# Optimization experiments

Measured on AMD Instinct MI355X. Metric: run time of the kernel, lower is better.

## Reference

```python
import jax, jax.numpy as jnp
import numpy as np

BATCH, T, VOCAB, HIDDEN = 32, 256, 8192, 1024
SCALE = 0.02  # small init so logits stay sane through the recurrence


def setup_inputs() -> dict:
    key = jax.random.key(0)
    ks = jax.random.split(key, 4)
    inputs = jax.random.normal(ks[0], (BATCH, T, VOCAB), dtype=jnp.float32)
    Wi = jax.random.normal(ks[1], (VOCAB, 4 * HIDDEN), dtype=jnp.float32) * SCALE
    Wh = jax.random.normal(ks[2], (HIDDEN, 4 * HIDDEN), dtype=jnp.float32) * SCALE
    bh = jnp.zeros((4 * HIDDEN,), dtype=jnp.float32)
    Wp = jax.random.normal(ks[3], (HIDDEN, VOCAB), dtype=jnp.float32) * SCALE
    bp = jnp.zeros((VOCAB,), dtype=jnp.float32)
    c0 = jnp.zeros((BATCH, HIDDEN), dtype=jnp.float32)
    h0 = jnp.zeros((BATCH, HIDDEN), dtype=jnp.float32)
    return {"inputs": inputs, "Wi": Wi, "Wh": Wh, "bh": bh,
            "Wp": Wp, "bp": bp, "c0": c0, "h0": h0}


def _decode(inputs, Wi, Wh, bh, Wp, bp, c0, h0, rng):
    vocab = inputs.shape[2]

    def step(carry, x_t):
        rng, c, h, last_pred = carry
        rng, cat_rng = jax.random.split(rng)
        x = last_pred  # teacher_force=False: feed back sampled one-hot token
        # fused LSTM gates (flax gate order i, f, g, o)
        z = x @ Wi + h @ Wh + bh  # [B, 4H]
        i, f, g, o = jnp.split(z, 4, axis=-1)
        c = jax.nn.sigmoid(f) * c + jax.nn.sigmoid(i) * jnp.tanh(g)
        h = jax.nn.sigmoid(o) * jnp.tanh(c)
        logits = h @ Wp + bp  # [B, V]
        tok = jax.random.categorical(cat_rng, logits)  # [B] int
        pred = jax.nn.one_hot(tok, vocab, dtype=jnp.float32)  # [B, V]
        return (rng, c, h, pred), (logits, pred)

    init = (rng, c0, h0, inputs[:, 0])
    xs = jnp.swapaxes(inputs, 0, 1)  # [T, B, V]
    _, (logits, preds) = jax.lax.scan(step, init, xs)
    # scan stacks on axis 0; original scan_in_dim puts time back on axis 1
    return jnp.swapaxes(logits, 0, 1), jnp.swapaxes(preds, 0, 1)


def reference(inputs, Wi, Wh, bh, Wp, bp, c0, h0):
    rng = jax.random.key(42)  # stands in for self.make_rng('lstm')
    return _decode(inputs, Wi, Wh, bh, Wp, bp, c0, h0, rng)
```

## Files before the change

### kernel.cpp

```cpp
#include <hip/hip_runtime.h>
#include <cstdint>
#include <cstddef>


namespace {

constexpr int BB = 32;
constexpr int TT = 256;
constexpr int VV = 8192;
constexpr int HH = 1024;
constexpr int ZC = 4096;
constexpr int NCOL = VV + ZC;
constexpr int K0S = 8;

__host__ __device__ inline uint32_t rotl(uint32_t v, int r) {
  return (v << r) | (v >> (32 - r));
}

__host__ __device__ inline void tf2x32(uint32_t k0, uint32_t k1,
                                       uint32_t x0, uint32_t x1,
                                       uint32_t &o0, uint32_t &o1) {
  const uint32_t ks2 = k0 ^ k1 ^ 0x1BD11BDAu;
  x0 += k0; x1 += k1;
#define R4A { x0+=x1; x1=rotl(x1,13); x1^=x0; x0+=x1; x1=rotl(x1,15); x1^=x0; \
              x0+=x1; x1=rotl(x1,26); x1^=x0; x0+=x1; x1=rotl(x1, 6); x1^=x0; }
#define R4B { x0+=x1; x1=rotl(x1,17); x1^=x0; x0+=x1; x1=rotl(x1,29); x1^=x0; \
              x0+=x1; x1=rotl(x1,16); x1^=x0; x0+=x1; x1=rotl(x1,24); x1^=x0; }
  R4A; x0 += k1;  x1 += ks2 + 1u;
  R4B; x0 += ks2; x1 += k0 + 2u;
  R4A; x0 += k0;  x1 += k1 + 3u;
  R4B; x0 += k1;  x1 += ks2 + 4u;
  R4A; x0 += ks2; x1 += k0 + 5u;
#undef R4A
#undef R4B
  o0 = x0; o1 = x1;
}

__device__ inline float sigf(float x) { return 1.0f / (1.0f + expf(-x)); }

__global__ __launch_bounds__(256) void k0_partial(
    const float* __restrict__ inputs,
    const float* __restrict__ h0,
    const float* __restrict__ Wi,
    const float* __restrict__ Wh,
    float* __restrict__ zpart0)
{
  const int cb = blockIdx.x % (ZC / 64);
  const int s  = blockIdx.x / (ZC / 64);
  const int c  = threadIdx.x & 63;
  const int w  = threadIdx.x >> 6;
  const int col = cb * 64 + c;
  const int u0 = s * 1152 + w * 288;

  float acc[BB];
#pragma unroll
  for (int b = 0; b < BB; ++b) acc[b] = 0.0f;

  for (int ui = 0; ui < 288; ++ui) {
    const int u = u0 + ui;
    const float wv = (u < VV) ? Wi[(size_t)u * ZC + col]
                              : Wh[(size_t)(u - VV) * ZC + col];
#pragma unroll
    for (int b = 0; b < BB; ++b) {
      const float a = (u < VV) ? inputs[(size_t)b * TT * VV + u]
                               : h0[b * HH + (u - VV)];
      acc[b] = fmaf(a, wv, acc[b]);
    }
  }

  __shared__ float red[4][BB][64];
#pragma unroll
  for (int b = 0; b < BB; ++b) red[w][b][c] = acc[b];
  __syncthreads();
  for (int i = threadIdx.x; i < BB * 64; i += 256) {
    const int b = i >> 6, cc = i & 63;
    const float s4 = red[0][b][cc] + red[1][b][cc] + red[2][b][cc] + red[3][b][cc];
    zpart0[((size_t)s * BB + b) * ZC + cb * 64 + cc] = s4;
  }
}

__global__ __launch_bounds__(256) void k0_reduce(
    const float* __restrict__ zpart0, const float* __restrict__ bh,
    float* __restrict__ zfull0)
{
  const int idx = blockIdx.x * 256 + threadIdx.x;
  const int b = idx / ZC, j = idx % ZC;
  float s = bh[j];
#pragma unroll
  for (int k = 0; k < K0S; ++k) s += zpart0[((size_t)k * BB + b) * ZC + j];
  zfull0[idx] = s;
}

template <int SPL>
__global__ __launch_bounds__(256) void k1_cell(
    const float* __restrict__ part,
    const float* __restrict__ zfull0,
    const float* __restrict__ bh,
    const float* __restrict__ Wi,
    const float* __restrict__ c0,
    const float* __restrict__ argval,
    const int*   __restrict__ argidx,
    float* __restrict__ cbuf, float* __restrict__ hbuf,
    float* __restrict__ preds_out,
    int t)
{
  const int b = blockIdx.x;
  __shared__ int tok_sh;
  if (t > 0) {
    if (threadIdx.x < 64) {
      const int lane = threadIdx.x;
      float v = -3.4e38f; int idx = 0x7fffffff;
      if (lane < 32) { v = argval[b * 32 + lane]; idx = argidx[b * 32 + lane]; }
#pragma unroll
      for (int off = 16; off; off >>= 1) {
        const float vo = __shfl_down(v, off);
        const int   io = __shfl_down(idx, off);
        if (vo > v || (vo == v && io < idx)) { v = vo; idx = io; }
      }
      if (lane == 0) tok_sh = idx;
    }
    __syncthreads();
  }
  const int tok = (t > 0) ? tok_sh : 0;
  if (t > 0 && threadIdx.x == 0) {
    preds_out[((size_t)b * TT + (t - 1)) * VV + tok] = 1.0f;
  }

  for (int u = threadIdx.x; u < HH; u += 256) {
    float zi, zf, zg, zo;
    if (t == 0) {
      const float* z0 = zfull0 + (size_t)b * ZC;
      zi = z0[u]; zf = z0[HH + u]; zg = z0[2 * HH + u]; zo = z0[3 * HH + u];
    } else {
      zi = bh[u]; zf = bh[HH + u]; zg = bh[2 * HH + u]; zo = bh[3 * HH + u];
#pragma unroll
      for (int s = 0; s < SPL; ++s) {
        const float* p = part + ((size_t)s * BB + b) * NCOL + VV;
        zi += p[u]; zf += p[HH + u]; zg += p[2 * HH + u]; zo += p[3 * HH + u];
      }
      const float* wrow = Wi + (size_t)tok * ZC;
      zi += wrow[u]; zf += wrow[HH + u]; zg += wrow[2 * HH + u]; zo += wrow[3 * HH + u];
    }
    const float cprev = (t == 0) ? c0[b * HH + u] : cbuf[b * HH + u];
    const float cc = sigf(zf) * cprev + sigf(zi) * tanhf(zg);
    const float hh = sigf(zo) * tanhf(cc);
    cbuf[b * HH + u] = cc;
    hbuf[b * HH + u] = hh;
  }
}

template <int SPL>
__global__ __launch_bounds__(256, 2) void kA(
    const float* __restrict__ hbuf,
    const float* __restrict__ Wp,
    const float* __restrict__ Wh,
    float* __restrict__ part)
{
  constexpr int UB  = HH / SPL;
  constexpr int UWH = UB / 2;
  constexpr int UC  = UWH / 8;
  constexpr int NCB = NCOL / 256;

  const int cb    = blockIdx.x % NCB;
  const int s     = blockIdx.x / NCB;
  const int lane  = threadIdx.x & 63;
  const int w     = threadIdx.x >> 6;
  const int uhalf = w >> 1;
  const int bhalf = w & 1;
  const int b0    = bhalf * 16;
  const int colbase = cb * 256;

  const float* W; int ldw, wcol0;
  if (colbase < VV) { W = Wp; ldw = VV; wcol0 = colbase + lane * 4; }
  else              { W = Wh; ldw = ZC; wcol0 = colbase - VV + lane * 4; }

  __shared__ __align__(16) float smem[BB * UB];

  const int u0 = s * UB;
  for (int f = threadIdx.x * 4; f < BB * UB; f += 1024) {
    const int b = f / UB, uu = f % UB;
    *(float4*)&smem[b * UB + uu] = *(const float4*)&hbuf[b * HH + u0 + uu];
  }
  __syncthreads();

  float4 acc[16];
#pragma unroll
  for (int i = 0; i < 16; ++i) acc[i] = make_float4(0.f, 0.f, 0.f, 0.f);

  const int uloc0 = uhalf * UWH;
  const float* wp = W + (size_t)(u0 + uloc0) * ldw + wcol0;

#pragma unroll 1
  for (int uc = 0; uc < UC; ++uc) {
    float4 wv[8];
#pragma unroll
    for (int k = 0; k < 8; ++k)
      wv[k] = *(const float4*)&wp[(size_t)(uc * 8 + k) * ldw];
#pragma unroll
    for (int bl = 0; bl < 16; ++bl) {
      const float* hrow = &smem[(b0 + bl) * UB + uloc0 + uc * 8];
      const float4 ha = *(const float4*)&hrow[0];
      const float4 hb = *(const float4*)&hrow[4];
      float4 a = acc[bl];
      a.x = fmaf(wv[0].x, ha.x, a.x); a.y = fmaf(wv[0].y, ha.x, a.y);
      a.z = fmaf(wv[0].z, ha.x, a.z); a.w = fmaf(wv[0].w, ha.x, a.w);
      a.x = fmaf(wv[1].x, ha.y, a.x); a.y = fmaf(wv[1].y, ha.y, a.y);
      a.z = fmaf(wv[1].z, ha.y, a.z); a.w = fmaf(wv[1].w, ha.y, a.w);
      a.x = fmaf(wv[2].x, ha.z, a.x); a.y = fmaf(wv[2].y, ha.z, a.y);
      a.z = fmaf(wv[2].z, ha.z, a.z); a.w = fmaf(wv[2].w, ha.z, a.w);
      a.x = fmaf(wv[3].x, ha.w, a.x); a.y = fmaf(wv[3].y, ha.w, a.y);
      a.z = fmaf(wv[3].z, ha.w, a.z); a.w = fmaf(wv[3].w, ha.w, a.w);
      a.x = fmaf(wv[4].x, hb.x, a.x); a.y = fmaf(wv[4].y, hb.x, a.y);
      a.z = fmaf(wv[4].z, hb.x, a.z); a.w = fmaf(wv[4].w, hb.x, a.w);
      a.x = fmaf(wv[5].x, hb.y, a.x); a.y = fmaf(wv[5].y, hb.y, a.y);
      a.z = fmaf(wv[5].z, hb.y, a.z); a.w = fmaf(wv[5].w, hb.y, a.w);
      a.x = fmaf(wv[6].x, hb.z, a.x); a.y = fmaf(wv[6].y, hb.z, a.y);
      a.z = fmaf(wv[6].z, hb.z, a.z); a.w = fmaf(wv[6].w, hb.z, a.w);
      a.x = fmaf(wv[7].x, hb.w, a.x); a.y = fmaf(wv[7].y, hb.w, a.y);
      a.z = fmaf(wv[7].z, hb.w, a.z); a.w = fmaf(wv[7].w, hb.w, a.w);
      acc[bl] = a;
    }
  }

  float4* red = (float4*)smem;
#pragma unroll
  for (int rb = 0; rb < 4; ++rb) {
    __syncthreads();
#pragma unroll
    for (int bl = 0; bl < 4; ++bl)
      red[((bhalf * 2 + uhalf) * 4 + bl) * 64 + lane] = acc[rb * 4 + bl];
    __syncthreads();
#pragma unroll
    for (int rep = 0; rep < 2; ++rep) {
      const int i  = rep * 256 + threadIdx.x;
      const int ln = i & 63, bl = (i >> 6) & 3, bh2 = i >> 8;
      const float4 r0 = red[((bh2 * 2 + 0) * 4 + bl) * 64 + ln];
      const float4 r1 = red[((bh2 * 2 + 1) * 4 + bl) * 64 + ln];
      float4 o;
      o.x = r0.x + r1.x; o.y = r0.y + r1.y;
      o.z = r0.z + r1.z; o.w = r0.w + r1.w;
      const int b = bh2 * 16 + rb * 4 + bl;
      *(float4*)&part[((size_t)s * BB + b) * NCOL + colbase + ln * 4] = o;
    }
  }
}

template <int SPL>
__global__ __launch_bounds__(256) void k3_logits(
    const float* __restrict__ part,
    const float* __restrict__ bp,
    float* __restrict__ logits_out,
    float* __restrict__ preds_out,
    float* __restrict__ argval, int* __restrict__ argidx,
    uint32_t ck0, uint32_t ck1, int t)
{
  const int b  = blockIdx.x >> 5;
  const int ch = blockIdx.x & 31;
  const int v  = ch * 256 + threadIdx.x;

  float lg = bp[v];
#pragma unroll
  for (int s = 0; s < SPL; ++s) lg += part[((size_t)s * BB + b) * NCOL + v];
  logits_out[((size_t)b * TT + t) * VV + v] = lg;
  preds_out [((size_t)b * TT + t) * VV + v] = 0.0f;

  const uint32_t j = (uint32_t)(b * VV + v);
  uint32_t r0, r1;
  tf2x32(ck0, ck1, 0u, j, r0, r1);
  const uint32_t bits = r0 ^ r1;
  const float u0 = __uint_as_float((bits >> 9) | 0x3f800000u) - 1.0f;
  const float uu = (u0 == 0.0f) ? 1.17549435e-38f : u0;
  const float g = -logf(-logf(uu));
  const float val = lg + g;

  __shared__ float sval[256];
  __shared__ int   sidx[256];
  sval[threadIdx.x] = val;
  sidx[threadIdx.x] = v;
  __syncthreads();
#pragma unroll
  for (int off = 128; off; off >>= 1) {
    if (threadIdx.x < off) {
      const float vo = sval[threadIdx.x + off];
      const int   io = sidx[threadIdx.x + off];
      if (vo > sval[threadIdx.x] ||
          (vo == sval[threadIdx.x] && io < sidx[threadIdx.x])) {
        sval[threadIdx.x] = vo; sidx[threadIdx.x] = io;
      }
    }
    __syncthreads();
  }
  if (threadIdx.x == 0) {
    argval[b * 32 + ch] = sval[0];
    argidx[b * 32 + ch] = sidx[0];
  }
}

__global__ __launch_bounds__(64) void kfinal(
    const float* __restrict__ argval, const int* __restrict__ argidx,
    float* __restrict__ preds_out)
{
  const int b = blockIdx.x, lane = threadIdx.x;
  float v = -3.4e38f; int idx = 0x7fffffff;
  if (lane < 32) { v = argval[b * 32 + lane]; idx = argidx[b * 32 + lane]; }
#pragma unroll
  for (int off = 16; off; off >>= 1) {
    const float vo = __shfl_down(v, off);
    const int   io = __shfl_down(idx, off);
    if (vo > v || (vo == v && io < idx)) { v = vo; idx = io; }
  }
  if (lane == 0) preds_out[((size_t)b * TT + (TT - 1)) * VV + idx] = 1.0f;
}

}

extern "C" void kernel_launch(void* const* d_in, const int* in_sizes, int n_in,
                              void* d_out, int out_size, void* d_ws, size_t ws_size,
                              hipStream_t stream) {
  const float* inputs = (const float*)d_in[0];
  const float* Wi     = (const float*)d_in[1];
  const float* Wh     = (const float*)d_in[2];
  const float* bh     = (const float*)d_in[3];
  const float* Wp     = (const float*)d_in[4];
  const float* bp     = (const float*)d_in[5];
  const float* c0     = (const float*)d_in[6];
  const float* h0     = (const float*)d_in[7];

  float* out_logits = (float*)d_out;
  float* out_preds  = out_logits + (size_t)BB * TT * VV;

  const size_t partB8 = (size_t)8 * BB * NCOL * sizeof(float);
  const size_t tailB  = ((size_t)BB * ZC + (size_t)BB * HH * 2 +
                         (size_t)BB * 32 * 2) * sizeof(float);
  const int spl = (ws_size >= partB8 + tailB + 1024) ? 8 : 4;
  const size_t partB = (size_t)spl * BB * NCOL * sizeof(float);

  uint8_t* ws = (uint8_t*)d_ws;
  float* part   = (float*)ws;
  float* zpart0 = (float*)ws;
  size_t off = partB;
  float* zfull0 = (float*)(ws + off); off += (size_t)BB * ZC * sizeof(float);
  float* cbuf   = (float*)(ws + off); off += (size_t)BB * HH * sizeof(float);
  float* hbuf   = (float*)(ws + off); off += (size_t)BB * HH * sizeof(float);
  float* argval = (float*)(ws + off); off += (size_t)BB * 32 * sizeof(float);
  int*   argidx = (int*)  (ws + off); off += (size_t)BB * 32 * sizeof(int);

  uint32_t k0 = 0u, k1 = 42u;
  uint32_t ck[TT][2];
  for (int t = 0; t < TT; ++t) {
    uint32_t a, b2; tf2x32(k0, k1, 0u, 1u, a, b2);
    ck[t][0] = a; ck[t][1] = b2;
    uint32_t n0, n1; tf2x32(k0, k1, 0u, 0u, n0, n1);
    k0 = n0; k1 = n1;
  }

  k0_partial<<<(ZC / 64) * K0S, 256, 0, stream>>>(inputs, h0, Wi, Wh, zpart0);
  k0_reduce<<<BB * ZC / 256, 256, 0, stream>>>(zpart0, bh, zfull0);

  for (int t = 0; t < TT; ++t) {
    if (spl == 8) {
      k1_cell<8><<<BB, 256, 0, stream>>>(part, zfull0, bh, Wi, c0, argval,
                                         argidx, cbuf, hbuf, out_preds, t);
      kA<8><<<(NCOL / 256) * 8, 256, 0, stream>>>(hbuf, Wp, Wh, part);
      k3_logits<8><<<BB * 32, 256, 0, stream>>>(part, bp, out_logits, out_preds,
                                                argval, argidx, ck[t][0], ck[t][1], t);
    } else {
      k1_cell<4><<<BB, 256, 0, stream>>>(part, zfull0, bh, Wi, c0, argval,
                                         argidx, cbuf, hbuf, out_preds, t);
      kA<4><<<(NCOL / 256) * 4, 256, 0, stream>>>(hbuf, Wp, Wh, part);
      k3_logits<4><<<BB * 32, 256, 0, stream>>>(part, bp, out_logits, out_preds,
                                                argval, argidx, ck[t][0], ck[t][1], t);
    }
  }
  kfinal<<<BB, 64, 0, stream>>>(argval, argidx, out_preds);
}
```

Baseline: 10.80 ms.

## Retile recurrent GEMV kernel to 128-column, 16-batch blocks with fixed 4-way split

The per-step matmul kernel is retiled so each block covers 128 columns and 16 batch rows over a 256-unit K slice, with a fixed K split of 4. This gives many more, smaller blocks (fewer accumulators per thread) and a single-pass reduction instead of four. Weight rows are now read twice, once per batch group, which raises L2/HBM weight traffic in exchange for more parallelism. The workspace-dependent split-8 path is removed.

```diff
diff --git a/kernel.cpp b/kernel.cpp
--- a/kernel.cpp
+++ b/kernel.cpp
@@ -11,6 +11,7 @@
 constexpr int HH = 1024;
 constexpr int ZC = 4096;
 constexpr int NCOL = VV + ZC;
+constexpr int SPL = 4;
 constexpr int K0S = 8;
 
 __host__ __device__ inline uint32_t rotl(uint32_t v, int r) {
@@ -91,7 +92,6 @@
   zfull0[idx] = s;
 }
 
-template <int SPL>
 __global__ __launch_bounds__(256) void k1_cell(
     const float* __restrict__ part,
     const float* __restrict__ zfull0,
@@ -149,56 +149,61 @@
   }
 }
 
-template <int SPL>
-__global__ __launch_bounds__(256, 2) void kA(
+__global__ __launch_bounds__(256) void kA(
     const float* __restrict__ hbuf,
     const float* __restrict__ Wp,
     const float* __restrict__ Wh,
     float* __restrict__ part)
 {
-  constexpr int UB  = HH / SPL;
-  constexpr int UWH = UB / 2;
-  constexpr int UC  = UWH / 8;
-  constexpr int NCB = NCOL / 256;
-
-  const int cb    = blockIdx.x % NCB;
-  const int s     = blockIdx.x / NCB;
-  const int lane  = threadIdx.x & 63;
-  const int w     = threadIdx.x >> 6;
-  const int uhalf = w >> 1;
-  const int bhalf = w & 1;
-  const int b0    = bhalf * 16;
-  const int colbase = cb * 256;
-
-  const float* W; int ldw, wcol0;
-  if (colbase < VV) { W = Wp; ldw = VV; wcol0 = colbase + lane * 4; }
-  else              { W = Wh; ldw = ZC; wcol0 = colbase - VV + lane * 4; }
-
-  __shared__ __align__(16) float smem[BB * UB];
-
-  const int u0 = s * UB;
-  for (int f = threadIdx.x * 4; f < BB * UB; f += 1024) {
-    const int b = f / UB, uu = f % UB;
-    *(float4*)&smem[b * UB + uu] = *(const float4*)&hbuf[b * HH + u0 + uu];
-  }
-  __syncthreads();
-
-  float4 acc[16];
-#pragma unroll
-  for (int i = 0; i < 16; ++i) acc[i] = make_float4(0.f, 0.f, 0.f, 0.f);
-
-  const int uloc0 = uhalf * UWH;
-  const float* wp = W + (size_t)(u0 + uloc0) * ldw + wcol0;
+  constexpr int NCB = NCOL / 128;
+  const int cb = blockIdx.x % NCB;
+  const int s  = (blockIdx.x / NCB) % SPL;
+  const int bg = blockIdx.x / (NCB * SPL);
+
+  const int tid     = threadIdx.x;
+  const int lane    = tid & 63;
+  const int w       = tid >> 6;
+  const int uhalf   = w >> 1;
+  const int bq      = w & 1;
+  const int lane_c  = lane & 31;
+  const int lane_bh = lane >> 5;
+  const int colbase = cb * 128;
+
+  const float* W; int ldw, wcol;
+  if (colbase < VV) { W = Wp; ldw = VV; wcol = colbase + lane_c * 4; }
+  else              { W = Wh; ldw = ZC; wcol = colbase - VV + lane_c * 4; }
+
+  __shared__ __align__(16) float smem[16 * 256];
+
+  const int u0 = s * 256;
+#pragma unroll
+  for (int k = 0; k < 4; ++k) {
+    const int j = tid + k * 256;
+    const int b = j >> 6;
+    const int uu = (j & 63) * 4;
+    *(float4*)&smem[b * 256 + uu] =
+        *(const float4*)&hbuf[(bg * 16 + b) * HH + u0 + uu];
+  }
+  __syncthreads();
+
+  float4 acc[4];
+#pragma unroll
+  for (int i = 0; i < 4; ++i) acc[i] = make_float4(0.f, 0.f, 0.f, 0.f);
+
+  const int bloc0 = bq * 8 + lane_bh * 4;
+  const float* wp = W + (size_t)(u0 + uhalf * 128) * ldw + wcol;
+  const float* hbase = &smem[bloc0 * 256 + uhalf * 128];
 
 #pragma unroll 1
-  for (int uc = 0; uc < UC; ++uc) {
+  for (int uc = 0; uc < 16; ++uc) {
     float4 wv[8];
 #pragma unroll
     for (int k = 0; k < 8; ++k)
-      wv[k] = *(const float4*)&wp[(size_t)(uc * 8 + k) * ldw];
-#pragma unroll
-    for (int bl = 0; bl < 16; ++bl) {
-      const float* hrow = &smem[(b0 + bl) * UB + uloc0 + uc * 8];
+      wv[k] = *(const float4*)&wp[(size_t)k * ldw];
+    wp += (size_t)8 * ldw;
+#pragma unroll
+    for (int bl = 0; bl < 4; ++bl) {
+      const float* hrow = hbase + bl * 256 + uc * 8;
       const float4 ha = *(const float4*)&hrow[0];
       const float4 hb = *(const float4*)&hrow[4];
       float4 a = acc[bl];
@@ -222,30 +227,26 @@
     }
   }
 
+  __syncthreads();
   float4* red = (float4*)smem;
 #pragma unroll
-  for (int rb = 0; rb < 4; ++rb) {
-    __syncthreads();
-#pragma unroll
-    for (int bl = 0; bl < 4; ++bl)
-      red[((bhalf * 2 + uhalf) * 4 + bl) * 64 + lane] = acc[rb * 4 + bl];
-    __syncthreads();
-#pragma unroll
-    for (int rep = 0; rep < 2; ++rep) {
-      const int i  = rep * 256 + threadIdx.x;
-      const int ln = i & 63, bl = (i >> 6) & 3, bh2 = i >> 8;
-      const float4 r0 = red[((bh2 * 2 + 0) * 4 + bl) * 64 + ln];
-      const float4 r1 = red[((bh2 * 2 + 1) * 4 + bl) * 64 + ln];
-      float4 o;
-      o.x = r0.x + r1.x; o.y = r0.y + r1.y;
-      o.z = r0.z + r1.z; o.w = r0.w + r1.w;
-      const int b = bh2 * 16 + rb * 4 + bl;
-      *(float4*)&part[((size_t)s * BB + b) * NCOL + colbase + ln * 4] = o;
-    }
-  }
-}
-
-template <int SPL>
+  for (int bl = 0; bl < 4; ++bl)
+    red[((bloc0 + bl) * 2 + uhalf) * 32 + lane_c] = acc[bl];
+  __syncthreads();
+#pragma unroll
+  for (int rep = 0; rep < 2; ++rep) {
+    const int i = rep * 256 + tid;
+    const int bl = i >> 5;
+    const int cq = i & 31;
+    const float4 r0 = red[(bl * 2 + 0) * 32 + cq];
+    const float4 r1 = red[(bl * 2 + 1) * 32 + cq];
+    float4 o;
+    o.x = r0.x + r1.x; o.y = r0.y + r1.y;
+    o.z = r0.z + r1.z; o.w = r0.w + r1.w;
+    *(float4*)&part[((size_t)s * BB + bg * 16 + bl) * NCOL + colbase + cq * 4] = o;
+  }
+}
+
 __global__ __launch_bounds__(256) void k3_logits(
     const float* __restrict__ part,
     const float* __restrict__ bp,
@@ -329,13 +330,8 @@
   float* out_logits = (float*)d_out;
   float* out_preds  = out_logits + (size_t)BB * TT * VV;
 
-  const size_t partB8 = (size_t)8 * BB * NCOL * sizeof(float);
-  const size_t tailB  = ((size_t)BB * ZC + (size_t)BB * HH * 2 +
-                         (size_t)BB * 32 * 2) * sizeof(float);
-  const int spl = (ws_size >= partB8 + tailB + 1024) ? 8 : 4;
-  const size_t partB = (size_t)spl * BB * NCOL * sizeof(float);
-
   uint8_t* ws = (uint8_t*)d_ws;
+  const size_t partB = (size_t)SPL * BB * NCOL * sizeof(float);
   float* part   = (float*)ws;
   float* zpart0 = (float*)ws;
   size_t off = partB;
@@ -358,19 +354,11 @@
   k0_reduce<<<BB * ZC / 256, 256, 0, stream>>>(zpart0, bh, zfull0);
 
   for (int t = 0; t < TT; ++t) {
-    if (spl == 8) {
-      k1_cell<8><<<BB, 256, 0, stream>>>(part, zfull0, bh, Wi, c0, argval,
-                                         argidx, cbuf, hbuf, out_preds, t);
-      kA<8><<<(NCOL / 256) * 8, 256, 0, stream>>>(hbuf, Wp, Wh, part);
-      k3_logits<8><<<BB * 32, 256, 0, stream>>>(part, bp, out_logits, out_preds,
-                                                argval, argidx, ck[t][0], ck[t][1], t);
-    } else {
-      k1_cell<4><<<BB, 256, 0, stream>>>(part, zfull0, bh, Wi, c0, argval,
-                                         argidx, cbuf, hbuf, out_preds, t);
-      kA<4><<<(NCOL / 256) * 4, 256, 0, stream>>>(hbuf, Wp, Wh, part);
-      k3_logits<4><<<BB * 32, 256, 0, stream>>>(part, bp, out_logits, out_preds,
-                                                argval, argidx, ck[t][0], ck[t][1], t);
-    }
+    k1_cell<<<BB, 256, 0, stream>>>(part, zfull0, bh, Wi, c0, argval,
+                                    argidx, cbuf, hbuf, out_preds, t);
+    kA<<<(NCOL / 128) * SPL * 2, 256, 0, stream>>>(hbuf, Wp, Wh, part);
+    k3_logits<<<BB * 32, 256, 0, stream>>>(part, bp, out_logits, out_preds,
+                                           argval, argidx, ck[t][0], ck[t][1], t);
   }
   kfinal<<<BB, 64, 0, stream>>>(argval, argidx, out_preds);
 }
```

Result: faster. 9.199 ms (-14.8%).
